# Optimization experiments

Hardware: AMD Instinct MI355X
Metric: run time of the kernel (lower is better)

Reference implementation:

```python
import jax, jax.numpy as jnp
import numpy as np

B, R, F, S, H, G, E, MH, A, TOPK = 2048, 39200, 512, 64, 512, 256, 32, 512, 7, 4


def _init(key, shape, scale=0.02):
    return (jax.random.normal(key, shape, dtype=jnp.float32) * scale).astype(jnp.float32)


def setup_inputs() -> dict:
    key = jax.random.key(0)
    ks = jax.random.split(key, 24)
    return {
        "obs": jax.random.normal(ks[0], (B, R), dtype=jnp.float32),
        "obs_sensor": jax.random.normal(ks[1], (B, S), dtype=jnp.float32),
        "std": jnp.ones((1,), dtype=jnp.float32),
        # trunk: Linear(R,F) + LayerNorm(F)
        "trunk_w": _init(ks[2], (R, F)),
        "trunk_b": jnp.zeros((F,), jnp.float32),
        "ln_g": jnp.ones((F,), jnp.float32),
        "ln_b": jnp.zeros((F,), jnp.float32),
        # policy1: Linear(F+S, H)
        "p1_w": _init(ks[3], (F + S, H)),
        "p1_b": jnp.zeros((H,), jnp.float32),
        # MoE gate MLP: Linear(H,G) -> ReLU -> Linear(G,E)
        "g_w1": _init(ks[4], (H, G)),
        "g_b1": jnp.zeros((G,), jnp.float32),
        "g_w2": _init(ks[5], (G, E)),
        "g_b2": jnp.zeros((E,), jnp.float32),
        # experts: per-expert MLP Linear(H,MH) -> ReLU -> Linear(MH,H)
        "e_w1": _init(ks[6], (E, H, MH)),
        "e_b1": jnp.zeros((E, MH), jnp.float32),
        "e_w2": _init(ks[7], (E, MH, H)),
        "e_b2": jnp.zeros((E, H), jnp.float32),
        # policy2: ReLU -> Linear(H, A)
        "p2_w": _init(ks[8], (H, A)),
        "p2_b": jnp.zeros((A,), jnp.float32),
    }


def _layernorm(x, g, b, eps=1e-5):
    mu = jnp.mean(x, axis=-1, keepdims=True)
    var = jnp.var(x, axis=-1, keepdims=True)
    return (x - mu) * jax.lax.rsqrt(var + eps) * g + b


def reference(obs, obs_sensor, std, trunk_w, trunk_b, ln_g, ln_b, p1_w, p1_b,
              g_w1, g_b1, g_w2, g_b2, e_w1, e_b1, e_w2, e_b2, p2_w, p2_b):
    # trunk
    h = jnp.tanh(_layernorm(obs @ trunk_w + trunk_b, ln_g, ln_b))
    h = jnp.concatenate([h, obs_sensor], axis=-1)
    # policy1
    x = jax.nn.relu(h @ p1_w + p1_b)  # [B, H]
    # MoE gating: top-k over softmax of gate-MLP logits
    logits = jax.nn.relu(x @ g_w1 + g_b1) @ g_w2 + g_b2  # [B, E]
    probs = jax.nn.softmax(logits, axis=-1)
    top_v, top_i = jax.lax.top_k(probs, TOPK)  # [B, K]
    w = top_v / jnp.sum(top_v, axis=-1, keepdims=True)
    rows = jnp.arange(x.shape[0])[:, None]
    gate_sparse = jnp.zeros_like(probs).at[rows, top_i].set(w)  # [B, E]
    mask = jnp.zeros_like(probs).at[rows, top_i].set(1.0)
    # expert compute (dense all-expert, weighted by sparse gate; dropout off in eval)
    hid = jax.nn.relu(jnp.einsum('bh,ehm->bem', x, e_w1) + e_b1)  # [B, E, MH]
    y = jnp.einsum('bem,emh->beh', hid, e_w2) + e_b2              # [B, E, H]
    x_moe = jnp.einsum('be,beh->bh', gate_sparse, y)              # [B, H]
    # load-balancing aux loss (Switch-style)
    density = jnp.mean(probs, axis=0)    # P_i
    frac = jnp.mean(mask, axis=0)        # f_i
    aux_loss = jnp.float32(E) * jnp.sum(frac * density)
    # policy2: ReLU -> Linear, then tanh
    mu = jnp.tanh(jax.nn.relu(x_moe) @ p2_w + p2_b)
    std_out = jnp.ones_like(mu) * std
    return (mu, std_out, aux_loss)
```

## Files before the change

### kernel.cpp

```cpp
#include <hip/hip_runtime.h>
#include <stdint.h>

typedef __attribute__((ext_vector_type(4))) float f32x4;
typedef __attribute__((ext_vector_type(8))) __bf16 bf16x8;
typedef unsigned short u16;
typedef u16 u16x8 __attribute__((ext_vector_type(8)));

#define DEV __device__ __forceinline__

DEV u16 f2bf(float f) {
  union { float f; uint32_t u; } v; v.f = f;
  uint32_t u = v.u;
  return (u16)((u + 0x7FFFu + ((u >> 16) & 1u)) >> 16);
}
DEV float bf2f(u16 h) {
  union { uint32_t u; float f; } v; v.u = ((uint32_t)h) << 16;
  return v.f;
}
DEV void async16(void* lds, const void* g) {
  __builtin_amdgcn_global_load_lds((const __attribute__((address_space(1))) void*)g,
                                   (__attribute__((address_space(3))) void*)lds, 16, 0, 0);
}

#define B_  2048
#define R_  39200
#define F_  512
#define S_  64
#define H_  512
#define G_  256
#define E_  32
#define MH_ 512
#define A_  7
#define KSLICES 35
#define KSLICE_LEN 1120

__global__ void transpose_bf16_kernel(const float* __restrict__ in, ushort* __restrict__ out,
                                      int R, int C) {
  __shared__ float tile[64][65];
  size_t bo = (size_t)blockIdx.z * R * C;
  const float* inp = in + bo;
  ushort* outp = out + bo;
  int r0 = blockIdx.y * 64, c0 = blockIdx.x * 64;
  int tid = threadIdx.x;
  {
    int rl = tid >> 2, cl = (tid & 3) * 16;
    if (r0 + rl < R) {
      const float4* src = (const float4*)(inp + (size_t)(r0 + rl) * C + c0 + cl);
#pragma unroll
      for (int j = 0; j < 4; j++) {
        float4 v = src[j];
        tile[rl][cl + 4 * j + 0] = v.x;
        tile[rl][cl + 4 * j + 1] = v.y;
        tile[rl][cl + 4 * j + 2] = v.z;
        tile[rl][cl + 4 * j + 3] = v.w;
      }
    }
  }
  __syncthreads();
  {
    int cl = tid >> 2, rl = (tid & 3) * 16;
    ushort* dst = outp + (size_t)(c0 + cl) * R + r0 + rl;
#pragma unroll
    for (int j = 0; j < 4; j++) {
      int rr = rl + 4 * j;
      if (r0 + rr < R) {
        ushort4 o;
        o.x = f2bf(tile[rr + 0][cl]);
        o.y = f2bf(tile[rr + 1][cl]);
        o.z = f2bf(tile[rr + 2][cl]);
        o.w = f2bf(tile[rr + 3][cl]);
        *(ushort4*)(dst + 4 * j) = o;
      }
    }
  }
}

__global__ __launch_bounds__(256)
void gemm_trunk_kernel(const float* __restrict__ A, const ushort* __restrict__ Bt,
                       float* __restrict__ Cp) {
  __shared__ __align__(16) ushort As[128 * 32];
  __shared__ __align__(16) ushort Bs[128 * 32];
  const int tid = threadIdx.x;
  const int w = tid >> 6, l = tid & 63;
  const int wm = w >> 1, wn = w & 1;
  const int lrow = l & 15, lq = l >> 4;
  const int mb = blockIdx.x >> 2, nb = blockIdx.x & 3;
  const int ks = blockIdx.y * KSLICE_LEN;
  f32x4 acc[4][4] = {};
  const int srow = tid >> 2, scol = (tid & 3) * 8;
  const ushort* Bb = Bt + (size_t)(nb * 128 + srow) * R_ + scol;
  char* BsB = (char*)Bs + w * 1024;
  const int arow = tid >> 1, acol = (tid & 1) * 16;
  const float* Ap = A + (size_t)(mb * 128 + arow) * R_ + acol;
  ushort* AsW = As + arow * 32 + acol;
  for (int k0 = ks; k0 < ks + KSLICE_LEN; k0 += 32) {
    async16(BsB,        Bb + k0);
    async16(BsB + 4096, Bb + (size_t)64 * R_ + k0);
    const float4* av = (const float4*)(Ap + k0);
    float4 f0 = av[0], f1 = av[1], f2 = av[2], f3 = av[3];
    u16x8 p0, p1;
    p0[0]=f2bf(f0.x); p0[1]=f2bf(f0.y); p0[2]=f2bf(f0.z); p0[3]=f2bf(f0.w);
    p0[4]=f2bf(f1.x); p0[5]=f2bf(f1.y); p0[6]=f2bf(f1.z); p0[7]=f2bf(f1.w);
    p1[0]=f2bf(f2.x); p1[1]=f2bf(f2.y); p1[2]=f2bf(f2.z); p1[3]=f2bf(f2.w);
    p1[4]=f2bf(f3.x); p1[5]=f2bf(f3.y); p1[6]=f2bf(f3.z); p1[7]=f2bf(f3.w);
    *(u16x8*)AsW       = p0;
    *(u16x8*)(AsW + 8) = p1;
    __syncthreads();
    bf16x8 af[4], bfr[4];
#pragma unroll
    for (int i = 0; i < 4; i++)
      af[i] = *(const bf16x8*)(As + (wm * 64 + i * 16 + lrow) * 32 + lq * 8);
#pragma unroll
    for (int i = 0; i < 4; i++)
      bfr[i] = *(const bf16x8*)(Bs + (wn * 64 + i * 16 + lrow) * 32 + lq * 8);
#pragma unroll
    for (int mi = 0; mi < 4; mi++)
#pragma unroll
      for (int ni = 0; ni < 4; ni++)
        acc[mi][ni] = __builtin_amdgcn_mfma_f32_16x16x32_bf16(af[mi], bfr[ni], acc[mi][ni], 0, 0, 0);
    __syncthreads();
  }
  float* C = Cp + (size_t)blockIdx.y * B_ * F_;
#pragma unroll
  for (int mi = 0; mi < 4; mi++)
#pragma unroll
    for (int ni = 0; ni < 4; ni++) {
      int col = nb * 128 + wn * 64 + ni * 16 + lrow;
#pragma unroll
      for (int r = 0; r < 4; r++) {
        int row = mb * 128 + wm * 64 + mi * 16 + lq * 4 + r;
        C[(size_t)row * F_ + col] = acc[mi][ni][r];
      }
    }
}

__global__ __launch_bounds__(256)
void gemm64_brelu_kernel(const ushort* __restrict__ A, const ushort* __restrict__ Bt,
                         const float* __restrict__ bias, ushort* __restrict__ out,
                         int K, int N, int nTiles) {
  __shared__ __align__(16) ushort As[64 * 32];
  __shared__ __align__(16) ushort Bs[64 * 32];
  const int tid = threadIdx.x;
  const int w = tid >> 6, l = tid & 63;
  const int wm = w >> 1, wn = w & 1;
  const int lrow = l & 15, lq = l >> 4;
  const int mb = blockIdx.x / nTiles, nb = blockIdx.x % nTiles;
  f32x4 acc[2][2] = {};
  const int srow = tid >> 2, scol = (tid & 3) * 8;
  const ushort* Ab = A + (size_t)(mb * 64 + srow) * K + scol;
  const ushort* Bb = Bt + (size_t)(nb * 64 + srow) * K + scol;
  char* AsB = (char*)As + w * 1024;
  char* BsB = (char*)Bs + w * 1024;
  for (int k0 = 0; k0 < K; k0 += 32) {
    async16(AsB, Ab + k0);
    async16(BsB, Bb + k0);
    __syncthreads();
    bf16x8 af[2], bfr[2];
#pragma unroll
    for (int i = 0; i < 2; i++)
      af[i] = *(const bf16x8*)(As + (wm * 32 + i * 16 + lrow) * 32 + lq * 8);
#pragma unroll
    for (int i = 0; i < 2; i++)
      bfr[i] = *(const bf16x8*)(Bs + (wn * 32 + i * 16 + lrow) * 32 + lq * 8);
#pragma unroll
    for (int mi = 0; mi < 2; mi++)
#pragma unroll
      for (int ni = 0; ni < 2; ni++)
        acc[mi][ni] = __builtin_amdgcn_mfma_f32_16x16x32_bf16(af[mi], bfr[ni], acc[mi][ni], 0, 0, 0);
    __syncthreads();
  }
#pragma unroll
  for (int mi = 0; mi < 2; mi++)
#pragma unroll
    for (int ni = 0; ni < 2; ni++) {
      int col = nb * 64 + wn * 32 + ni * 16 + lrow;
      float bv = bias[col];
#pragma unroll
      for (int r = 0; r < 4; r++) {
        int row = mb * 64 + wm * 32 + mi * 16 + lq * 4 + r;
        out[(size_t)row * N + col] = f2bf(fmaxf(acc[mi][ni][r] + bv, 0.f));
      }
    }
}

__global__ void reduce_ln_kernel(const float* __restrict__ Cp, const float* __restrict__ tb,
                                 const float* __restrict__ g, const float* __restrict__ bb,
                                 const float* __restrict__ sensor, ushort* __restrict__ xcat) {
  int row = blockIdx.x, tid = threadIdx.x;
  const float* base = Cp + (size_t)row * F_;
  float v0 = tb[tid], v1 = tb[tid + 256];
#pragma unroll
  for (int s = 0; s < KSLICES; s++) {
    v0 += base[(size_t)s * B_ * F_ + tid];
    v1 += base[(size_t)s * B_ * F_ + tid + 256];
  }
  float s1 = v0 + v1, s2 = v0 * v0 + v1 * v1;
  for (int o = 32; o; o >>= 1) { s1 += __shfl_down(s1, o); s2 += __shfl_down(s2, o); }
  __shared__ float r1[4], r2[4];
  __shared__ float mus, rss;
  if ((tid & 63) == 0) { r1[tid >> 6] = s1; r2[tid >> 6] = s2; }
  __syncthreads();
  if (tid == 0) {
    float a = r1[0] + r1[1] + r1[2] + r1[3];
    float q = r2[0] + r2[1] + r2[2] + r2[3];
    float mu = a * (1.0f / F_);
    float var = q * (1.0f / F_) - mu * mu;
    mus = mu; rss = rsqrtf(var + 1e-5f);
  }
  __syncthreads();
  float mu = mus, rs = rss;
  ushort* xr = xcat + (size_t)row * (F_ + S_);
  xr[tid]       = f2bf(tanhf((v0 - mu) * rs * g[tid] + bb[tid]));
  xr[tid + 256] = f2bf(tanhf((v1 - mu) * rs * g[tid + 256] + bb[tid + 256]));
  if (tid < S_) xr[F_ + tid] = f2bf(sensor[(size_t)row * S_ + tid]);
}

__global__ void gate_topk_kernel(const ushort* __restrict__ tbuf, const float* __restrict__ w2,
                                 const float* __restrict__ b2, float* __restrict__ gate_w,
                                 int* __restrict__ gate_i, float* __restrict__ density,
                                 int* __restrict__ counts) {
  int row = blockIdx.x, tid = threadIdx.x;
  __shared__ float trs[G_];
  const ushort* tr = tbuf + (size_t)row * G_;
  if (tid < 64) {
    ushort4 v = ((const ushort4*)tr)[tid];
    trs[tid * 4 + 0] = bf2f(v.x);
    trs[tid * 4 + 1] = bf2f(v.y);
    trs[tid * 4 + 2] = bf2f(v.z);
    trs[tid * 4 + 3] = bf2f(v.w);
  }
  __syncthreads();
  int jj = tid >> 5, e = tid & 31;
  float s = 0;
  int k0 = jj * 32;
#pragma unroll
  for (int k = 0; k < 32; k++) s += trs[k0 + k] * w2[(size_t)(k0 + k) * E_ + e];
  __shared__ float part[8][32];
  part[jj][e] = s;
  __syncthreads();
  if (tid < 32) {
    float logit = b2[tid];
#pragma unroll
    for (int j = 0; j < 8; j++) logit += part[j][tid];
    float m = logit;
    for (int o = 16; o; o >>= 1) m = fmaxf(m, __shfl_xor(m, o));
    float p = expf(logit - m);
    float sum = p;
    for (int o = 16; o; o >>= 1) sum += __shfl_xor(sum, o);
    float prob = p / sum;
    bool sel = false;
    float tv[4]; int ti[4];
#pragma unroll
    for (int it = 0; it < 4; it++) {
      float c = sel ? -1.0f : prob;
      float mx = c;
      for (int o = 16; o; o >>= 1) mx = fmaxf(mx, __shfl_xor(mx, o));
      unsigned long long bal = __ballot(c == mx);
      int idx = __ffsll(bal) - 1;
      if (tid == idx) sel = true;
      tv[it] = mx; ti[it] = idx;
    }
    float wsum = tv[0] + tv[1] + tv[2] + tv[3];
#pragma unroll
    for (int it = 0; it < 4; it++)
      if (tid == it) { gate_w[row * 4 + it] = tv[it] / wsum; gate_i[row * 4 + it] = ti[it]; }
    atomicAdd(&density[tid], prob);
    if (sel) atomicAdd(&counts[tid], 1);
  }
}

__global__ void scan_aux_kernel(const int* __restrict__ counts, const float* __restrict__ density,
                                int* __restrict__ offsets, float* __restrict__ aux_out) {
  if (threadIdx.x == 0) {
    int acc = 0; float a = 0;
    for (int e = 0; e < E_; e++) {
      offsets[e] = acc; acc += counts[e];
      a += (float)counts[e] * density[e];
    }
    aux_out[0] = (float)E_ * a / ((float)B_ * (float)B_);
  }
}

__global__ void fill_slots_kernel(const int* __restrict__ gate_i, const float* __restrict__ gate_w,
                                  const int* __restrict__ offsets, int* __restrict__ cursors,
                                  int* __restrict__ slot_row, float* __restrict__ slot_w) {
  int r = blockIdx.x * blockDim.x + threadIdx.x;
  if (r >= B_) return;
  for (int k = 0; k < 4; k++) {
    int e = gate_i[r * 4 + k];
    int pos = atomicAdd(&cursors[e], 1);
    int s = offsets[e] + pos;
    slot_row[s] = r;
    slot_w[s] = gate_w[r * 4 + k];
  }
}

__global__ __launch_bounds__(256)
void expert1_kernel(const ushort* __restrict__ x, const ushort* __restrict__ w1T,
                    const float* __restrict__ b1, const int* __restrict__ counts,
                    const int* __restrict__ offsets, const int* __restrict__ slot_row,
                    ushort* __restrict__ hid) {
  const int e = blockIdx.z, nb = blockIdx.y, cx = blockIdx.x;
  const int cnt = counts[e];
  if (cnt == 0) return;
  const int off = offsets[e];
  __shared__ __align__(16) ushort As[64 * 32];
  __shared__ __align__(16) ushort Bs[128 * 32];
  const int tid = threadIdx.x;
  const int w = tid >> 6, l = tid & 63;
  const int wm = w >> 1, wn = w & 1;
  const int lrow = l & 15, lq = l >> 4;
  const int srow = tid >> 2, scol = (tid & 3) * 8;
  const ushort* Wb = w1T + (size_t)e * H_ * MH_ + (size_t)(nb * 128 + srow) * H_ + scol;
  char* AsB = (char*)As + w * 1024;
  char* BsB = (char*)Bs + w * 1024;
  for (int base = cx * 64; base < cnt; base += 64 * 8) {
    int sl = base + srow; if (sl > cnt - 1) sl = cnt - 1;
    const ushort* Ab = x + (size_t)slot_row[off + sl] * H_ + scol;
    f32x4 acc[2][4] = {};
    for (int k0 = 0; k0 < H_; k0 += 32) {
      async16(AsB,        Ab + k0);
      async16(BsB,        Wb + k0);
      async16(BsB + 4096, Wb + (size_t)64 * H_ + k0);
      __syncthreads();
      bf16x8 af[2], bfr[4];
#pragma unroll
      for (int i = 0; i < 2; i++)
        af[i] = *(const bf16x8*)(As + (wm * 32 + i * 16 + lrow) * 32 + lq * 8);
#pragma unroll
      for (int i = 0; i < 4; i++)
        bfr[i] = *(const bf16x8*)(Bs + (wn * 64 + i * 16 + lrow) * 32 + lq * 8);
#pragma unroll
      for (int mi = 0; mi < 2; mi++)
#pragma unroll
        for (int ni = 0; ni < 4; ni++)
          acc[mi][ni] = __builtin_amdgcn_mfma_f32_16x16x32_bf16(af[mi], bfr[ni], acc[mi][ni], 0, 0, 0);
      __syncthreads();
    }
    int mrem = cnt - base;
#pragma unroll
    for (int mi = 0; mi < 2; mi++)
#pragma unroll
      for (int ni = 0; ni < 4; ni++) {
        int col = nb * 128 + wn * 64 + ni * 16 + lrow;
        float bv = b1[e * MH_ + col];
#pragma unroll
        for (int r = 0; r < 4; r++) {
          int rl = wm * 32 + mi * 16 + lq * 4 + r;
          if (rl < mrem)
            hid[(size_t)(off + base + rl) * MH_ + col] = f2bf(fmaxf(acc[mi][ni][r] + bv, 0.f));
        }
      }
  }
}

__global__ __launch_bounds__(256)
void expert2_kernel(const ushort* __restrict__ hid, const ushort* __restrict__ w2T,
                    const float* __restrict__ b2, const int* __restrict__ counts,
                    const int* __restrict__ offsets, const int* __restrict__ slot_row,
                    const float* __restrict__ slot_w, float* __restrict__ xmoe) {
  const int e = blockIdx.z, nb = blockIdx.y, cx = blockIdx.x;
  const int cnt = counts[e];
  if (cnt == 0) return;
  const int off = offsets[e];
  __shared__ __align__(16) ushort As[64 * 32];
  __shared__ __align__(16) ushort Bs[128 * 32];
  const int tid = threadIdx.x;
  const int w = tid >> 6, l = tid & 63;
  const int wm = w >> 1, wn = w & 1;
  const int lrow = l & 15, lq = l >> 4;
  const int srow = tid >> 2, scol = (tid & 3) * 8;
  const ushort* Wb = w2T + (size_t)e * MH_ * H_ + (size_t)(nb * 128 + srow) * MH_ + scol;
  char* AsB = (char*)As + w * 1024;
  char* BsB = (char*)Bs + w * 1024;
  for (int base = cx * 64; base < cnt; base += 64 * 8) {
    int sl = base + srow; if (sl > cnt - 1) sl = cnt - 1;
    const ushort* Ab = hid + (size_t)(off + sl) * MH_ + scol;
    f32x4 acc[2][4] = {};
    for (int k0 = 0; k0 < MH_; k0 += 32) {
      async16(AsB,        Ab + k0);
      async16(BsB,        Wb + k0);
      async16(BsB + 4096, Wb + (size_t)64 * MH_ + k0);
      __syncthreads();
      bf16x8 af[2], bfr[4];
#pragma unroll
      for (int i = 0; i < 2; i++)
        af[i] = *(const bf16x8*)(As + (wm * 32 + i * 16 + lrow) * 32 + lq * 8);
#pragma unroll
      for (int i = 0; i < 4; i++)
        bfr[i] = *(const bf16x8*)(Bs + (wn * 64 + i * 16 + lrow) * 32 + lq * 8);
#pragma unroll
      for (int mi = 0; mi < 2; mi++)
#pragma unroll
        for (int ni = 0; ni < 4; ni++)
          acc[mi][ni] = __builtin_amdgcn_mfma_f32_16x16x32_bf16(af[mi], bfr[ni], acc[mi][ni], 0, 0, 0);
      __syncthreads();
    }
    int mrem = cnt - base;
#pragma unroll
    for (int mi = 0; mi < 2; mi++)
#pragma unroll
      for (int ni = 0; ni < 4; ni++) {
        int col = nb * 128 + wn * 64 + ni * 16 + lrow;
        float bv = b2[e * H_ + col];
#pragma unroll
        for (int r = 0; r < 4; r++) {
          int rl = wm * 32 + mi * 16 + lq * 4 + r;
          if (rl < mrem) {
            int s = off + base + rl;
            atomicAdd(&xmoe[(size_t)slot_row[s] * H_ + col], slot_w[s] * (acc[mi][ni][r] + bv));
          }
        }
      }
  }
}

__global__ void policy2_kernel(const float* __restrict__ xm, const float* __restrict__ w,
                               const float* __restrict__ b, const float* __restrict__ stdp,
                               float* __restrict__ out) {
  int l = threadIdx.x & 63;
  int row = blockIdx.x * 4 + (threadIdx.x >> 6);
  const float* xr = xm + (size_t)row * H_;
  const float4* x4 = (const float4*)(xr + l * 8);
  float4 a0 = x4[0], a1 = x4[1];
  float v[8] = {a0.x, a0.y, a0.z, a0.w, a1.x, a1.y, a1.z, a1.w};
#pragma unroll
  for (int j = 0; j < 8; j++) v[j] = fmaxf(v[j], 0.f);
  float res[7];
#pragma unroll
  for (int a = 0; a < A_; a++) {
    float s = 0;
#pragma unroll
    for (int j = 0; j < 8; j++) s += v[j] * w[(size_t)(l * 8 + j) * A_ + a];
    for (int o = 32; o; o >>= 1) s += __shfl_down(s, o);
    res[a] = s;
  }
  if (l == 0) {
    float sv = stdp[0];
#pragma unroll
    for (int a = 0; a < A_; a++) {
      out[(size_t)row * A_ + a] = tanhf(res[a] + b[a]);
      out[(size_t)B_ * A_ + (size_t)row * A_ + a] = sv;
    }
  }
}

extern "C" void kernel_launch(void* const* d_in, const int* in_sizes, int n_in,
                              void* d_out, int out_size, void* d_ws, size_t ws_size,
                              hipStream_t stream) {
  const float* obs      = (const float*)d_in[0];
  const float* sensor   = (const float*)d_in[1];
  const float* stdp     = (const float*)d_in[2];
  const float* trunk_w  = (const float*)d_in[3];
  const float* trunk_b  = (const float*)d_in[4];
  const float* ln_g     = (const float*)d_in[5];
  const float* ln_b     = (const float*)d_in[6];
  const float* p1_w     = (const float*)d_in[7];
  const float* p1_b     = (const float*)d_in[8];
  const float* g_w1     = (const float*)d_in[9];
  const float* g_b1     = (const float*)d_in[10];
  const float* g_w2     = (const float*)d_in[11];
  const float* g_b2     = (const float*)d_in[12];
  const float* e_w1     = (const float*)d_in[13];
  const float* e_b1     = (const float*)d_in[14];
  const float* e_w2     = (const float*)d_in[15];
  const float* e_b2     = (const float*)d_in[16];
  const float* p2_w     = (const float*)d_in[17];
  const float* p2_b     = (const float*)d_in[18];
  float* out = (float*)d_out;

  char* ws = (char*)d_ws;
  size_t off = 0;
  auto alloc = [&](size_t bytes) -> char* {
    char* p = ws + off;
    off += (bytes + 255) & ~(size_t)255;
    return p;
  };
  ushort* wT      = (ushort*)alloc((size_t)F_ * R_ * 2);
  float*  partial = (float*) alloc((size_t)KSLICES * B_ * F_ * 4);
  ushort* xcat    = (ushort*)alloc((size_t)B_ * (F_ + S_) * 2);
  ushort* p1T     = (ushort*)alloc((size_t)H_ * (F_ + S_) * 2);
  ushort* xbuf    = (ushort*)alloc((size_t)B_ * H_ * 2);
  ushort* g1T     = (ushort*)alloc((size_t)G_ * H_ * 2);
  ushort* tbuf    = (ushort*)alloc((size_t)B_ * G_ * 2);
  ushort* ew1T    = (ushort*)alloc((size_t)E_ * H_ * MH_ * 2);
  ushort* ew2T    = (ushort*)alloc((size_t)E_ * MH_ * H_ * 2);
  ushort* hid     = (ushort*)alloc(((size_t)B_ * 4 + 64) * MH_ * 2);
  float*  xmoe    = (float*) alloc((size_t)B_ * H_ * 4);
  float*  gate_w  = (float*) alloc((size_t)B_ * 4 * 4);
  int*    gate_i  = (int*)   alloc((size_t)B_ * 4 * 4);
  int*    counts  = (int*)   alloc(E_ * 4);
  int*    offsets = (int*)   alloc(E_ * 4);
  int*    cursors = (int*)   alloc(E_ * 4);
  float*  density = (float*) alloc(E_ * 4);
  int*    slot_row= (int*)   alloc((size_t)B_ * 4 * 4);
  float*  slot_w  = (float*) alloc((size_t)B_ * 4 * 4);

  hipMemsetAsync(counts, 0, E_ * 4, stream);
  hipMemsetAsync(cursors, 0, E_ * 4, stream);
  hipMemsetAsync(density, 0, E_ * 4, stream);
  hipMemsetAsync(xmoe, 0, (size_t)B_ * H_ * 4, stream);

  transpose_bf16_kernel<<<dim3(F_/64, (R_+63)/64, 1),   dim3(256), 0, stream>>>(trunk_w, wT, R_, F_);
  transpose_bf16_kernel<<<dim3(H_/64, (F_+S_)/64, 1),   dim3(256), 0, stream>>>(p1_w, p1T, F_ + S_, H_);
  transpose_bf16_kernel<<<dim3(G_/64, H_/64, 1),        dim3(256), 0, stream>>>(g_w1, g1T, H_, G_);
  transpose_bf16_kernel<<<dim3(MH_/64, H_/64, E_),      dim3(256), 0, stream>>>(e_w1, ew1T, H_, MH_);
  transpose_bf16_kernel<<<dim3(H_/64, MH_/64, E_),      dim3(256), 0, stream>>>(e_w2, ew2T, MH_, H_);

  gemm_trunk_kernel<<<dim3(64, KSLICES), 256, 0, stream>>>(obs, wT, partial);
  reduce_ln_kernel<<<B_, 256, 0, stream>>>(partial, trunk_b, ln_g, ln_b, sensor, xcat);

  gemm64_brelu_kernel<<<32 * 8, 256, 0, stream>>>(xcat, p1T, p1_b, xbuf, F_ + S_, H_, 8);
  gemm64_brelu_kernel<<<32 * 4, 256, 0, stream>>>(xbuf, g1T, g_b1, tbuf, H_, G_, 4);
  gate_topk_kernel<<<B_, 256, 0, stream>>>(tbuf, g_w2, g_b2, gate_w, gate_i, density, counts);
  scan_aux_kernel<<<1, 64, 0, stream>>>(counts, density, offsets, out + 2 * B_ * A_);
  fill_slots_kernel<<<8, 256, 0, stream>>>(gate_i, gate_w, offsets, cursors, slot_row, slot_w);

  expert1_kernel<<<dim3(8, 4, E_), 256, 0, stream>>>(xbuf, ew1T, e_b1, counts, offsets, slot_row, hid);
  expert2_kernel<<<dim3(8, 4, E_), 256, 0, stream>>>(hid, ew2T, e_b2, counts, offsets, slot_row, slot_w, xmoe);

  policy2_kernel<<<B_ / 4, 256, 0, stream>>>(xmoe, p2_w, p2_b, stdp, out);
}
```

Before: 985.8 us.

## Merge transposes, use atomic split-K trunk GEMM with wider tiles, fuse scan/fill

Five weight-transpose launches become one multi-job kernel. The trunk GEMM moves to 512-thread blocks with 128x256 tiles and accumulates split-K partials into one buffer with unsafe float atomics. That removes the 35-slice partial buffer and the heavy reduction inside the LayerNorm kernel. The scan and slot-fill kernels are merged into one block using LDS cursors, and memsets are consolidated. In exchange it adds atomic contention, non-deterministic summation order, and unsafe atomics that may behave differently on fine-grained memory.

```diff
diff --git a/kernel.cpp b/kernel.cpp
--- a/kernel.cpp
+++ b/kernel.cpp
@@ -4,7 +4,6 @@
 typedef __attribute__((ext_vector_type(4))) float f32x4;
 typedef __attribute__((ext_vector_type(8))) __bf16 bf16x8;
 typedef unsigned short u16;
-typedef u16 u16x8 __attribute__((ext_vector_type(8)));
 
 #define DEV __device__ __forceinline__
 
@@ -34,13 +33,25 @@
 #define KSLICES 35
 #define KSLICE_LEN 1120
 
-__global__ void transpose_bf16_kernel(const float* __restrict__ in, ushort* __restrict__ out,
-                                      int R, int C) {
+struct TJob { const float* in; ushort* out; int R, C, tilesX, tilesPerZ, off; };
+struct TJobs { TJob j[5]; };
+
+__global__ void multi_transpose_kernel(TJobs jobs) {
   __shared__ float tile[64][65];
-  size_t bo = (size_t)blockIdx.z * R * C;
-  const float* inp = in + bo;
-  ushort* outp = out + bo;
-  int r0 = blockIdx.y * 64, c0 = blockIdx.x * 64;
+  int bx = blockIdx.x;
+  int ji = 0;
+#pragma unroll
+  for (int k = 1; k < 5; k++) if (bx >= jobs.j[k].off) ji = k;
+  TJob jb = jobs.j[ji];
+  int lin = bx - jb.off;
+  int z = lin / jb.tilesPerZ;
+  int rem = lin - z * jb.tilesPerZ;
+  int tX = rem % jb.tilesX;
+  int tY = rem / jb.tilesX;
+  const float* inp = jb.in + (size_t)z * jb.R * jb.C;
+  ushort* outp = jb.out + (size_t)z * jb.R * jb.C;
+  int r0 = tY * 64, c0 = tX * 64;
+  int R = jb.R, C = jb.C;
   int tid = threadIdx.x;
   {
     int rl = tid >> 2, cl = (tid & 3) * 16;
@@ -75,36 +86,37 @@
   }
 }
 
-__global__ __launch_bounds__(256)
+__global__ __launch_bounds__(512, 4)
 void gemm_trunk_kernel(const float* __restrict__ A, const ushort* __restrict__ Bt,
-                       float* __restrict__ Cp) {
+                       float* __restrict__ C) {
   __shared__ __align__(16) ushort As[128 * 32];
-  __shared__ __align__(16) ushort Bs[128 * 32];
+  __shared__ __align__(16) ushort Bs[256 * 32];
   const int tid = threadIdx.x;
   const int w = tid >> 6, l = tid & 63;
-  const int wm = w >> 1, wn = w & 1;
+  const int wm = w >> 2, wn = w & 3;
   const int lrow = l & 15, lq = l >> 4;
-  const int mb = blockIdx.x >> 2, nb = blockIdx.x & 3;
+  const int mb = blockIdx.x >> 1, nb = blockIdx.x & 1;
   const int ks = blockIdx.y * KSLICE_LEN;
   f32x4 acc[4][4] = {};
   const int srow = tid >> 2, scol = (tid & 3) * 8;
-  const ushort* Bb = Bt + (size_t)(nb * 128 + srow) * R_ + scol;
+  const ushort* Bb0 = Bt + (size_t)(nb * 256 + srow) * R_ + scol;
+  const ushort* Bb1 = Bb0 + (size_t)128 * R_;
   char* BsB = (char*)Bs + w * 1024;
-  const int arow = tid >> 1, acol = (tid & 1) * 16;
-  const float* Ap = A + (size_t)(mb * 128 + arow) * R_ + acol;
-  ushort* AsW = As + arow * 32 + acol;
+  const int ar = tid >> 3, ac = (tid & 7) * 4;
+  const float* Ap0 = A + (size_t)(mb * 128 + ar) * R_ + ac;
+  const float* Ap1 = Ap0 + (size_t)64 * R_;
+  ushort* AsW0 = As + ar * 32 + ac;
+  ushort* AsW1 = AsW0 + 64 * 32;
   for (int k0 = ks; k0 < ks + KSLICE_LEN; k0 += 32) {
-    async16(BsB,        Bb + k0);
-    async16(BsB + 4096, Bb + (size_t)64 * R_ + k0);
-    const float4* av = (const float4*)(Ap + k0);
-    float4 f0 = av[0], f1 = av[1], f2 = av[2], f3 = av[3];
-    u16x8 p0, p1;
-    p0[0]=f2bf(f0.x); p0[1]=f2bf(f0.y); p0[2]=f2bf(f0.z); p0[3]=f2bf(f0.w);
-    p0[4]=f2bf(f1.x); p0[5]=f2bf(f1.y); p0[6]=f2bf(f1.z); p0[7]=f2bf(f1.w);
-    p1[0]=f2bf(f2.x); p1[1]=f2bf(f2.y); p1[2]=f2bf(f2.z); p1[3]=f2bf(f2.w);
-    p1[4]=f2bf(f3.x); p1[5]=f2bf(f3.y); p1[6]=f2bf(f3.z); p1[7]=f2bf(f3.w);
-    *(u16x8*)AsW       = p0;
-    *(u16x8*)(AsW + 8) = p1;
+    async16(BsB,        Bb0 + k0);
+    async16(BsB + 8192, Bb1 + k0);
+    float4 f0 = *(const float4*)(Ap0 + k0);
+    float4 f1 = *(const float4*)(Ap1 + k0);
+    ushort4 p0, p1;
+    p0.x = f2bf(f0.x); p0.y = f2bf(f0.y); p0.z = f2bf(f0.z); p0.w = f2bf(f0.w);
+    p1.x = f2bf(f1.x); p1.y = f2bf(f1.y); p1.z = f2bf(f1.z); p1.w = f2bf(f1.w);
+    *(ushort4*)AsW0 = p0;
+    *(ushort4*)AsW1 = p1;
     __syncthreads();
     bf16x8 af[4], bfr[4];
 #pragma unroll
@@ -120,18 +132,44 @@
         acc[mi][ni] = __builtin_amdgcn_mfma_f32_16x16x32_bf16(af[mi], bfr[ni], acc[mi][ni], 0, 0, 0);
     __syncthreads();
   }
-  float* C = Cp + (size_t)blockIdx.y * B_ * F_;
 #pragma unroll
   for (int mi = 0; mi < 4; mi++)
 #pragma unroll
     for (int ni = 0; ni < 4; ni++) {
-      int col = nb * 128 + wn * 64 + ni * 16 + lrow;
+      int col = nb * 256 + wn * 64 + ni * 16 + lrow;
 #pragma unroll
       for (int r = 0; r < 4; r++) {
         int row = mb * 128 + wm * 64 + mi * 16 + lq * 4 + r;
-        C[(size_t)row * F_ + col] = acc[mi][ni][r];
+        unsafeAtomicAdd(&C[(size_t)row * F_ + col], acc[mi][ni][r]);
       }
     }
+}
+
+__global__ void ln_kernel(const float* __restrict__ C, const float* __restrict__ tb,
+                          const float* __restrict__ g, const float* __restrict__ bb,
+                          const float* __restrict__ sensor, ushort* __restrict__ xcat) {
+  int row = blockIdx.x, tid = threadIdx.x;
+  float v0 = C[(size_t)row * F_ + tid] + tb[tid];
+  float v1 = C[(size_t)row * F_ + tid + 256] + tb[tid + 256];
+  float s1 = v0 + v1, s2 = v0 * v0 + v1 * v1;
+  for (int o = 32; o; o >>= 1) { s1 += __shfl_down(s1, o); s2 += __shfl_down(s2, o); }
+  __shared__ float r1[4], r2[4];
+  __shared__ float mus, rss;
+  if ((tid & 63) == 0) { r1[tid >> 6] = s1; r2[tid >> 6] = s2; }
+  __syncthreads();
+  if (tid == 0) {
+    float a = r1[0] + r1[1] + r1[2] + r1[3];
+    float q = r2[0] + r2[1] + r2[2] + r2[3];
+    float mu = a * (1.0f / F_);
+    float var = q * (1.0f / F_) - mu * mu;
+    mus = mu; rss = rsqrtf(var + 1e-5f);
+  }
+  __syncthreads();
+  float mu = mus, rs = rss;
+  ushort* xr = xcat + (size_t)row * (F_ + S_);
+  xr[tid]       = f2bf(tanhf((v0 - mu) * rs * g[tid] + bb[tid]));
+  xr[tid + 256] = f2bf(tanhf((v1 - mu) * rs * g[tid + 256] + bb[tid + 256]));
+  if (tid < S_) xr[F_ + tid] = f2bf(sensor[(size_t)row * S_ + tid]);
 }
 
 __global__ __launch_bounds__(256)
@@ -183,38 +221,6 @@
     }
 }
 
-__global__ void reduce_ln_kernel(const float* __restrict__ Cp, const float* __restrict__ tb,
-                                 const float* __restrict__ g, const float* __restrict__ bb,
-                                 const float* __restrict__ sensor, ushort* __restrict__ xcat) {
-  int row = blockIdx.x, tid = threadIdx.x;
-  const float* base = Cp + (size_t)row * F_;
-  float v0 = tb[tid], v1 = tb[tid + 256];
-#pragma unroll
-  for (int s = 0; s < KSLICES; s++) {
-    v0 += base[(size_t)s * B_ * F_ + tid];
-    v1 += base[(size_t)s * B_ * F_ + tid + 256];
-  }
-  float s1 = v0 + v1, s2 = v0 * v0 + v1 * v1;
-  for (int o = 32; o; o >>= 1) { s1 += __shfl_down(s1, o); s2 += __shfl_down(s2, o); }
-  __shared__ float r1[4], r2[4];
-  __shared__ float mus, rss;
-  if ((tid & 63) == 0) { r1[tid >> 6] = s1; r2[tid >> 6] = s2; }
-  __syncthreads();
-  if (tid == 0) {
-    float a = r1[0] + r1[1] + r1[2] + r1[3];
-    float q = r2[0] + r2[1] + r2[2] + r2[3];
-    float mu = a * (1.0f / F_);
-    float var = q * (1.0f / F_) - mu * mu;
-    mus = mu; rss = rsqrtf(var + 1e-5f);
-  }
-  __syncthreads();
-  float mu = mus, rs = rss;
-  ushort* xr = xcat + (size_t)row * (F_ + S_);
-  xr[tid]       = f2bf(tanhf((v0 - mu) * rs * g[tid] + bb[tid]));
-  xr[tid + 256] = f2bf(tanhf((v1 - mu) * rs * g[tid + 256] + bb[tid + 256]));
-  if (tid < S_) xr[F_ + tid] = f2bf(sensor[(size_t)row * S_ + tid]);
-}
-
 __global__ void gate_topk_kernel(const ushort* __restrict__ tbuf, const float* __restrict__ w2,
                                  const float* __restrict__ b2, float* __restrict__ gate_w,
                                  int* __restrict__ gate_i, float* __restrict__ density,
@@ -269,29 +275,32 @@
   }
 }
 
-__global__ void scan_aux_kernel(const int* __restrict__ counts, const float* __restrict__ density,
-                                int* __restrict__ offsets, float* __restrict__ aux_out) {
-  if (threadIdx.x == 0) {
+__global__ void scan_fill_kernel(const int* __restrict__ counts, const float* __restrict__ density,
+                                 const int* __restrict__ gate_i, const float* __restrict__ gate_w,
+                                 int* __restrict__ offsets, int* __restrict__ slot_row,
+                                 float* __restrict__ slot_w, float* __restrict__ aux_out) {
+  __shared__ int soff[E_];
+  __shared__ int scur[E_];
+  int tid = threadIdx.x;
+  if (tid < E_) scur[tid] = 0;
+  if (tid == 0) {
     int acc = 0; float a = 0;
     for (int e = 0; e < E_; e++) {
-      offsets[e] = acc; acc += counts[e];
+      soff[e] = acc; offsets[e] = acc; acc += counts[e];
       a += (float)counts[e] * density[e];
     }
     aux_out[0] = (float)E_ * a / ((float)B_ * (float)B_);
   }
-}
-
-__global__ void fill_slots_kernel(const int* __restrict__ gate_i, const float* __restrict__ gate_w,
-                                  const int* __restrict__ offsets, int* __restrict__ cursors,
-                                  int* __restrict__ slot_row, float* __restrict__ slot_w) {
-  int r = blockIdx.x * blockDim.x + threadIdx.x;
-  if (r >= B_) return;
-  for (int k = 0; k < 4; k++) {
-    int e = gate_i[r * 4 + k];
-    int pos = atomicAdd(&cursors[e], 1);
-    int s = offsets[e] + pos;
-    slot_row[s] = r;
-    slot_w[s] = gate_w[r * 4 + k];
+  __syncthreads();
+  for (int r = tid; r < B_; r += blockDim.x) {
+#pragma unroll
+    for (int k = 0; k < 4; k++) {
+      int e = gate_i[r * 4 + k];
+      int pos = atomicAdd(&scur[e], 1);
+      int s = soff[e] + pos;
+      slot_row[s] = r;
+      slot_w[s] = gate_w[r * 4 + k];
+    }
   }
 }
 
@@ -408,7 +417,7 @@
           int rl = wm * 32 + mi * 16 + lq * 4 + r;
           if (rl < mrem) {
             int s = off + base + rl;
-            atomicAdd(&xmoe[(size_t)slot_row[s] * H_ + col], slot_w[s] * (acc[mi][ni][r] + bv));
+            unsafeAtomicAdd(&xmoe[(size_t)slot_row[s] * H_ + col], slot_w[s] * (acc[mi][ni][r] + bv));
           }
         }
       }
@@ -477,7 +486,8 @@
     return p;
   };
   ushort* wT      = (ushort*)alloc((size_t)F_ * R_ * 2);
-  float*  partial = (float*) alloc((size_t)KSLICES * B_ * F_ * 4);
+  float*  Cbuf    = (float*) alloc((size_t)B_ * F_ * 4);
+  float*  xmoe    = (float*) alloc((size_t)B_ * H_ * 4);
   ushort* xcat    = (ushort*)alloc((size_t)B_ * (F_ + S_) * 2);
   ushort* p1T     = (ushort*)alloc((size_t)H_ * (F_ + S_) * 2);
   ushort* xbuf    = (ushort*)alloc((size_t)B_ * H_ * 2);
@@ -486,35 +496,38 @@
   ushort* ew1T    = (ushort*)alloc((size_t)E_ * H_ * MH_ * 2);
   ushort* ew2T    = (ushort*)alloc((size_t)E_ * MH_ * H_ * 2);
   ushort* hid     = (ushort*)alloc(((size_t)B_ * 4 + 64) * MH_ * 2);
-  float*  xmoe    = (float*) alloc((size_t)B_ * H_ * 4);
+  int*    counts  = (int*)   alloc(E_ * 4);
+  float*  density = (float*) alloc(E_ * 4);
+  int*    offsets = (int*)   alloc(E_ * 4);
   float*  gate_w  = (float*) alloc((size_t)B_ * 4 * 4);
   int*    gate_i  = (int*)   alloc((size_t)B_ * 4 * 4);
-  int*    counts  = (int*)   alloc(E_ * 4);
-  int*    offsets = (int*)   alloc(E_ * 4);
-  int*    cursors = (int*)   alloc(E_ * 4);
-  float*  density = (float*) alloc(E_ * 4);
   int*    slot_row= (int*)   alloc((size_t)B_ * 4 * 4);
   float*  slot_w  = (float*) alloc((size_t)B_ * 4 * 4);
 
-  hipMemsetAsync(counts, 0, E_ * 4, stream);
-  hipMemsetAsync(cursors, 0, E_ * 4, stream);
-  hipMemsetAsync(density, 0, E_ * 4, stream);
-  hipMemsetAsync(xmoe, 0, (size_t)B_ * H_ * 4, stream);
-
-  transpose_bf16_kernel<<<dim3(F_/64, (R_+63)/64, 1),   dim3(256), 0, stream>>>(trunk_w, wT, R_, F_);
-  transpose_bf16_kernel<<<dim3(H_/64, (F_+S_)/64, 1),   dim3(256), 0, stream>>>(p1_w, p1T, F_ + S_, H_);
-  transpose_bf16_kernel<<<dim3(G_/64, H_/64, 1),        dim3(256), 0, stream>>>(g_w1, g1T, H_, G_);
-  transpose_bf16_kernel<<<dim3(MH_/64, H_/64, E_),      dim3(256), 0, stream>>>(e_w1, ew1T, H_, MH_);
-  transpose_bf16_kernel<<<dim3(H_/64, MH_/64, E_),      dim3(256), 0, stream>>>(e_w2, ew2T, MH_, H_);
-
-  gemm_trunk_kernel<<<dim3(64, KSLICES), 256, 0, stream>>>(obs, wT, partial);
-  reduce_ln_kernel<<<B_, 256, 0, stream>>>(partial, trunk_b, ln_g, ln_b, sensor, xcat);
+  hipMemsetAsync(counts, 0, 512, stream);
+  hipMemsetAsync(Cbuf, 0, (size_t)(B_ * F_ + B_ * H_) * 4, stream);
+
+  TJobs jobs;
+  jobs.j[0] = { trunk_w, wT,   R_,      F_, F_ / 64,      ((R_ + 63) / 64) * (F_ / 64), 0 };
+  int o1 = jobs.j[0].tilesPerZ;
+  jobs.j[1] = { p1_w,    p1T,  F_ + S_, H_, H_ / 64,      ((F_ + S_) / 64) * (H_ / 64), o1 };
+  int o2 = o1 + jobs.j[1].tilesPerZ;
+  jobs.j[2] = { g_w1,    g1T,  H_,      G_, G_ / 64,      (H_ / 64) * (G_ / 64),        o2 };
+  int o3 = o2 + jobs.j[2].tilesPerZ;
+  jobs.j[3] = { e_w1,    ew1T, H_,      MH_, MH_ / 64,    (H_ / 64) * (MH_ / 64),       o3 };
+  int o4 = o3 + E_ * jobs.j[3].tilesPerZ;
+  jobs.j[4] = { e_w2,    ew2T, MH_,     H_, H_ / 64,      (MH_ / 64) * (H_ / 64),       o4 };
+  int total = o4 + E_ * jobs.j[4].tilesPerZ;
+  multi_transpose_kernel<<<total, 256, 0, stream>>>(jobs);
+
+  gemm_trunk_kernel<<<dim3(32, KSLICES), 512, 0, stream>>>(obs, wT, Cbuf);
+  ln_kernel<<<B_, 256, 0, stream>>>(Cbuf, trunk_b, ln_g, ln_b, sensor, xcat);
 
   gemm64_brelu_kernel<<<32 * 8, 256, 0, stream>>>(xcat, p1T, p1_b, xbuf, F_ + S_, H_, 8);
   gemm64_brelu_kernel<<<32 * 4, 256, 0, stream>>>(xbuf, g1T, g_b1, tbuf, H_, G_, 4);
   gate_topk_kernel<<<B_, 256, 0, stream>>>(tbuf, g_w2, g_b2, gate_w, gate_i, density, counts);
-  scan_aux_kernel<<<1, 64, 0, stream>>>(counts, density, offsets, out + 2 * B_ * A_);
-  fill_slots_kernel<<<8, 256, 0, stream>>>(gate_i, gate_w, offsets, cursors, slot_row, slot_w);
+  scan_fill_kernel<<<1, 1024, 0, stream>>>(counts, density, gate_i, gate_w, offsets,
+                                           slot_row, slot_w, out + 2 * B_ * A_);
 
   expert1_kernel<<<dim3(8, 4, E_), 256, 0, stream>>>(xbuf, ew1T, e_b1, counts, offsets, slot_row, hid);
   expert2_kernel<<<dim3(8, 4, E_), 256, 0, stream>>>(hid, ew2T, e_b2, counts, offsets, slot_row, slot_w, xmoe);
```

New measurement: 969.7 us. No clear change (-1.6%).
